# Performance work log

Hardware: AMD Instinct MI355X
Metric: run time of the kernel (lower is better)

The kernel has to match this reference:

```python
import jax, jax.numpy as jnp
import numpy as np

EPS = 1e-6

def _rmsnorm(x, w):
    # x: [..., Dh]
    inv = jax.lax.rsqrt(jnp.mean(x * x, axis=-1, keepdims=True) + EPS)
    return x * inv * w

def _apply_rope(x, rope):
    # x: [B, H, L, Dh], rope: [L, Dh//2, 2]
    L = x.shape[-2]
    cos = rope[:L, :, 0]  # [L, Dh//2]
    sin = rope[:L, :, 1]
    x_even = x[..., 0::2]
    x_odd = x[..., 1::2]
    rot = jnp.stack([x_even * cos - x_odd * sin,
                     x_even * sin + x_odd * cos], axis=-1)  # [B,H,L,Dh//2,2]
    return rot.reshape(*x.shape[:-1], -1)


def setup_inputs() -> dict:
    key = jax.random.key(0)
    ks = jax.random.split(key, 4)
    B, L, D = 2, 2048, 1024
    H, Dh = 16, 64
    x = jax.random.normal(ks[0], (B, L, D), dtype=jnp.float32)
    rope = jax.random.normal(ks[1], (L, Dh // 2, 2), dtype=jnp.float32)
    w_qkv = jax.random.normal(ks[2], (3 * D, D), dtype=jnp.float32) * (1.0 / np.sqrt(D))
    w_proj = jax.random.normal(ks[3], (D, D), dtype=jnp.float32) * (1.0 / np.sqrt(D))
    q_norm_w = jnp.ones((Dh,), dtype=jnp.float32)
    k_norm_w = jnp.ones((Dh,), dtype=jnp.float32)
    return {"x": x, "rope": rope, "w_qkv": w_qkv, "w_proj": w_proj,
            "q_norm_w": q_norm_w, "k_norm_w": k_norm_w}


def reference(x, rope, w_qkv, w_proj, q_norm_w, k_norm_w):
    B, L, D = x.shape
    H = 16
    Dh = D // H
    qkv = jnp.einsum('bld,ed->ble', x, w_qkv).reshape(B, L, 3, H, Dh)
    qkv = jnp.transpose(qkv, (2, 0, 3, 1, 4))  # [3, B, H, L, Dh]
    q, k, v = qkv[0], qkv[1], qkv[2]
    q = _rmsnorm(q, q_norm_w)
    k = _rmsnorm(k, k_norm_w)
    q = _apply_rope(q, rope)
    k = _apply_rope(k, rope)
    scale = 1.0 / np.sqrt(Dh)
    scores = jnp.einsum('bhqd,bhkd->bhqk', q, k) * scale
    attn = jax.nn.softmax(scores, axis=-1)
    out = jnp.einsum('bhqk,bhkd->bhqd', attn, v)  # [B,H,L,Dh]
    out = jnp.transpose(out, (0, 2, 1, 3)).reshape(B, L, D)
    return jnp.einsum('bld,ed->ble', out, w_proj)
```

## Files before the change

### kernel.cpp

```cpp
#include <hip/hip_runtime.h>

typedef unsigned short u16;
typedef unsigned int u32;
typedef __bf16 bf16x8 __attribute__((ext_vector_type(8)));
typedef float f32x4 __attribute__((ext_vector_type(4)));

#define L_SEQ 2048
#define NH 16
#define DH 64
#define D_MODEL 1024
#define ATT_SHIFT2 14.426950408889634f

__device__ __forceinline__ u16 f2bf(float f) {
  union { float f; u32 u; } v; v.f = f;
  u32 u = v.u;
  return (u16)((u + 0x7fffu + ((u >> 16) & 1u)) >> 16);
}
__device__ __forceinline__ float bf2f(u16 b) {
  union { u32 u; float f; } v; v.u = ((u32)b) << 16;
  return v.f;
}
__device__ __forceinline__ u32 pk2(float lo_val, float hi_val) {
  union { float f; u32 u; } a, b;
  a.f = hi_val; b.f = lo_val;
  return __builtin_amdgcn_perm(a.u + 0x8000u, b.u + 0x8000u, 0x07060302u);
}
__device__ __forceinline__ u32 pk2t(float lo_val, float hi_val) {
  union { float f; u32 u; } a, b;
  a.f = hi_val; b.f = lo_val;
  return __builtin_amdgcn_perm(a.u, b.u, 0x07060302u);
}
__device__ __forceinline__ bf16x8 ld8(const u16* p) {
  union { uint4 u; bf16x8 b; } v;
  v.u = *(const uint4*)p;
  return v.b;
}
__device__ __forceinline__ f32x4 fzero4() { f32x4 z = {0.f, 0.f, 0.f, 0.f}; return z; }

__device__ __forceinline__ float fexp2(float x) {
#if __has_builtin(__builtin_amdgcn_exp2f)
  return __builtin_amdgcn_exp2f(x);
#else
  return __expf(x * 0.6931471805599453f);
#endif
}

__device__ __forceinline__ void gll16(const u16* g, u16* l) {
  __builtin_amdgcn_global_load_lds((const __attribute__((address_space(1))) u32*)g,
                                   (__attribute__((address_space(3))) u32*)l, 16, 0, 0);
}

__global__ __launch_bounds__(256) void cvt_all(const float* __restrict__ x,
                                               const float* __restrict__ wqkv,
                                               const float* __restrict__ wproj,
                                               u16* __restrict__ xb,
                                               u16* __restrict__ wqkvb,
                                               u16* __restrict__ wprojb) {
  int i = blockIdx.x * 256 + threadIdx.x;
  const float* s;
  u16* d;
  int off;
  if (i < 1048576)      { s = x;     d = xb;     off = i; }
  else if (i < 1835008) { s = wqkv;  d = wqkvb;  off = i - 1048576; }
  else                  { s = wproj; d = wprojb; off = i - 1835008; }
  float4 v = ((const float4*)s)[off];
  ((ushort4*)d)[off] = make_ushort4(f2bf(v.x), f2bf(v.y), f2bf(v.z), f2bf(v.w));
}

__global__ __launch_bounds__(256) void gemm_qkv(const u16* __restrict__ A,
                                                const u16* __restrict__ B,
                                                u16* __restrict__ qb,
                                                u16* __restrict__ kb,
                                                u16* __restrict__ vtb) {
  __shared__ u16 smem[16384];
  u16* As = smem;
  u16* Bs = smem + 8192;
  const int t = threadIdx.x;
  const int lane = t & 63, wv = t >> 6;
  const int col = lane & 15, quad = lane >> 4;
  const int wr = wv >> 1, wc = wv & 1;
  const int m0 = blockIdx.y * 128, n0 = blockIdx.x * 128;

  f32x4 acc[4][4];
#pragma unroll
  for (int i = 0; i < 4; ++i)
#pragma unroll
    for (int j = 0; j < 4; ++j) acc[i][j] = fzero4();

  for (int kt = 0; kt < 1024; kt += 64) {
    __syncthreads();
#pragma unroll
    for (int it = 0; it < 4; ++it) {
      int id0 = it * 256 + wv * 64;
      int id = id0 + lane;
      int row = id >> 3, cs = id & 7;
      int csrc = cs ^ (row & 7);
      gll16(A + (size_t)(m0 + row) * 1024 + kt + csrc * 8, As + (size_t)id0 * 8);
      gll16(B + (size_t)(n0 + row) * 1024 + kt + csrc * 8, Bs + (size_t)id0 * 8);
    }
    __syncthreads();
#pragma unroll
    for (int c = 0; c < 2; ++c) {
      bf16x8 af[4], bfv[4];
#pragma unroll
      for (int f = 0; f < 4; ++f) {
        int r = wr * 64 + f * 16 + col;
        af[f] = ld8(&As[(r * 8 + ((c * 4 + quad) ^ (r & 7))) * 8]);
        int rb = wc * 64 + f * 16 + col;
        bfv[f] = ld8(&Bs[(rb * 8 + ((c * 4 + quad) ^ (rb & 7))) * 8]);
      }
#pragma unroll
      for (int i = 0; i < 4; ++i)
#pragma unroll
        for (int j = 0; j < 4; ++j)
          acc[i][j] = __builtin_amdgcn_mfma_f32_16x16x32_bf16(af[i], bfv[j], acc[i][j], 0, 0, 0);
    }
  }

  const int region = n0 >> 10;
  if (region < 2) {
    u16* dst = region ? kb : qb;
#pragma unroll
    for (int i = 0; i < 4; ++i) {
      int gr = m0 + wr * 64 + i * 16 + quad * 4;
      int b = gr >> 11, l = gr & 2047;
#pragma unroll
      for (int j = 0; j < 4; ++j) {
        int gc = (n0 & 1023) + wc * 64 + j * 16 + col;
        int h = gc >> 6, dh = gc & 63;
        size_t base = ((size_t)(b * NH + h) * L_SEQ + l) * DH + dh;
#pragma unroll
        for (int r = 0; r < 4; ++r)
          dst[base + (size_t)r * DH] = f2bf(acc[i][j][r]);
      }
    }
  } else {
    __syncthreads();
#pragma unroll
    for (int i = 0; i < 4; ++i) {
      int m_l = wr * 64 + i * 16 + quad * 4;
#pragma unroll
      for (int j = 0; j < 4; ++j) {
        int n_l = wc * 64 + j * 16 + col;
        int ta = n_l * 128 + (m_l ^ ((n_l & 15) << 3));
        *(uint2*)(smem + ta) = make_uint2(pk2(acc[i][j][0], acc[i][j][1]),
                                          pk2(acc[i][j][2], acc[i][j][3]));
      }
    }
    __syncthreads();
    const int b = m0 >> 11, lbase = m0 & 2047;
    const int n_l = t >> 1, mh = (t & 1) * 64;
    const int gc = (n0 - 2048) + n_l;
    const int h = gc >> 6, dh = gc & 63;
    u16* vrow = vtb + ((size_t)(b * NH + h) * DH + dh) * L_SEQ + lbase + mh;
#pragma unroll
    for (int c2 = 0; c2 < 8; ++c2) {
      int m = mh + c2 * 8;
      uint4 v = *(const uint4*)(smem + n_l * 128 + (m ^ ((n_l & 15) << 3)));
      *(uint4*)(vrow + c2 * 8) = v;
    }
  }
}

__global__ __launch_bounds__(256) void qk_norm_rope(u16* __restrict__ qb,
                                                    u16* __restrict__ kb,
                                                    const float* __restrict__ rope,
                                                    const float* __restrict__ qw,
                                                    const float* __restrict__ kw) {
  const int t = threadIdx.x;
  const int lane = t & 63, wv = t >> 6;
  const int gid = blockIdx.x * 4 + wv;
  const int l = gid & (L_SEQ - 1);
  const int b = gid >> 11;
  const int lg = lane & 7;
  const float QSCALE = 0.125f * 1.4426950408889634f;

  float wqv[8], wkv[8], rp[8];
  {
    float4 a = *(const float4*)(qw + lg * 8);
    float4 c = *(const float4*)(qw + lg * 8 + 4);
    wqv[0]=a.x; wqv[1]=a.y; wqv[2]=a.z; wqv[3]=a.w; wqv[4]=c.x; wqv[5]=c.y; wqv[6]=c.z; wqv[7]=c.w;
    a = *(const float4*)(kw + lg * 8);
    c = *(const float4*)(kw + lg * 8 + 4);
    wkv[0]=a.x; wkv[1]=a.y; wkv[2]=a.z; wkv[3]=a.w; wkv[4]=c.x; wkv[5]=c.y; wkv[6]=c.z; wkv[7]=c.w;
    a = *(const float4*)(rope + (size_t)l * 64 + lg * 8);
    c = *(const float4*)(rope + (size_t)l * 64 + lg * 8 + 4);
    rp[0]=a.x; rp[1]=a.y; rp[2]=a.z; rp[3]=a.w; rp[4]=c.x; rp[5]=c.y; rp[6]=c.z; rp[7]=c.w;
  }

#pragma unroll
  for (int i = 0; i < 2; ++i) {
    const int head = i * 8 + (lane >> 3);
    size_t addr = ((size_t)(b * NH + head) * L_SEQ + l) * DH + lg * 8;
    bf16x8 q8 = ld8(qb + addr);
    bf16x8 k8 = ld8(kb + addr);
    float q[8], k[8];
#pragma unroll
    for (int j = 0; j < 8; ++j) { q[j] = (float)q8[j]; k[j] = (float)k8[j]; }
    float sq = 0.f, sk = 0.f;
#pragma unroll
    for (int j = 0; j < 8; ++j) { sq += q[j] * q[j]; sk += k[j] * k[j]; }
    sq += __shfl_xor(sq, 1); sq += __shfl_xor(sq, 2); sq += __shfl_xor(sq, 4);
    sk += __shfl_xor(sk, 1); sk += __shfl_xor(sk, 2); sk += __shfl_xor(sk, 4);
    float qi = rsqrtf(sq * (1.f / 64.f) + 1e-6f);
    float ki = rsqrtf(sk * (1.f / 64.f) + 1e-6f);

    float rq[8], rk[8];
#pragma unroll
    for (int j = 0; j < 4; ++j) {
      float cs = rp[2 * j], sn = rp[2 * j + 1];
      float qe = q[2 * j] * qi * wqv[2 * j], qo = q[2 * j + 1] * qi * wqv[2 * j + 1];
      float ke = k[2 * j] * ki * wkv[2 * j], ko = k[2 * j + 1] * ki * wkv[2 * j + 1];
      rq[2 * j]     = (qe * cs - qo * sn) * QSCALE;
      rq[2 * j + 1] = (qe * sn + qo * cs) * QSCALE;
      rk[2 * j]     = ke * cs - ko * sn;
      rk[2 * j + 1] = ke * sn + ko * cs;
    }
    *(uint4*)(qb + addr) = make_uint4(pk2(rq[0], rq[1]), pk2(rq[2], rq[3]),
                                      pk2(rq[4], rq[5]), pk2(rq[6], rq[7]));
    *(uint4*)(kb + addr) = make_uint4(pk2(rk[0], rk[1]), pk2(rk[2], rk[3]),
                                      pk2(rk[4], rk[5]), pk2(rk[6], rk[7]));
  }
}

__global__ __launch_bounds__(256) void attn_flash(const u16* __restrict__ qb,
                                                  const u16* __restrict__ kb,
                                                  const u16* __restrict__ vtb,
                                                  u16* __restrict__ po,
                                                  float* __restrict__ pl) {
  __shared__ u16 ldsK[4096];
  __shared__ u16 ldsV[4096];
  __shared__ u16 ldsP[8192];
  const int t = threadIdx.x;
  const int lane = t & 63, wv = t >> 6;
  const int col = lane & 15, quad = lane >> 4;
  const int bh = blockIdx.x;
  const int half = blockIdx.z;
  const int q0 = blockIdx.y * 128 + wv * 32;

  const u16* kbase = kb + ((size_t)bh * L_SEQ + half * 1024) * DH;
  const u16* vbase = vtb + (size_t)bh * DH * L_SEQ + half * 1024;

  bf16x8 qfrag[2][2];
#pragma unroll
  for (int qf = 0; qf < 2; ++qf)
#pragma unroll
    for (int c = 0; c < 2; ++c)
      qfrag[qf][c] = ld8(qb + ((size_t)bh * L_SEQ + q0 + qf * 16 + col) * DH + c * 32 + quad * 8);

  f32x4 o[2][4];
#pragma unroll
  for (int qf = 0; qf < 2; ++qf)
#pragma unroll
    for (int nf = 0; nf < 4; ++nf) o[qf][nf] = fzero4();
  float lrow[2] = {0.f, 0.f};

  u16* pb = &ldsP[wv * 2048];

  for (int tt = 0; tt < 16; ++tt) {
    __syncthreads();
    {
      const int kt = tt * 64;
#pragma unroll
      for (int it = 0; it < 2; ++it) {
        int id0 = it * 256 + wv * 64;
        int id = id0 + lane;
        int row = id >> 3, cs = id & 7, csrc = cs ^ (row & 7);
        gll16(kbase + (size_t)(kt + row) * DH + csrc * 8, ldsK + (size_t)id0 * 8);
        gll16(vbase + (size_t)row * L_SEQ + kt + csrc * 8, ldsV + (size_t)id0 * 8);
      }
    }
    __syncthreads();

    f32x4 s[2][4];
#pragma unroll
    for (int qf = 0; qf < 2; ++qf)
#pragma unroll
      for (int mf = 0; mf < 4; ++mf) s[qf][mf] = fzero4();
#pragma unroll
    for (int c = 0; c < 2; ++c) {
#pragma unroll
      for (int mf = 0; mf < 4; ++mf) {
        int kr = mf * 16 + col;
        bf16x8 kf = ld8(&ldsK[kr * 64 + (((c * 4 + quad) ^ (kr & 7)) * 8)]);
#pragma unroll
        for (int qf = 0; qf < 2; ++qf)
          s[qf][mf] = __builtin_amdgcn_mfma_f32_16x16x32_bf16(kf, qfrag[qf][c], s[qf][mf], 0, 0, 0);
      }
    }

#pragma unroll
    for (int qf = 0; qf < 2; ++qf) {
      float ts = 0.f;
#pragma unroll
      for (int mf = 0; mf < 4; ++mf)
#pragma unroll
        for (int r = 0; r < 4; ++r) {
          float e = fexp2(s[qf][mf][r] - ATT_SHIFT2);
          s[qf][mf][r] = e;
          ts += e;
        }
      lrow[qf] += ts;
      const int q = qf * 16 + col;
#pragma unroll
      for (int mf = 0; mf < 4; ++mf) {
        int slot = q * 8 + ((2 * mf + (quad >> 1)) ^ (q & 7));
        *(uint2*)(pb + slot * 8 + (quad & 1) * 4) =
            make_uint2(pk2t(s[qf][mf][0], s[qf][mf][1]), pk2t(s[qf][mf][2], s[qf][mf][3]));
      }
    }

#pragma unroll
    for (int c = 0; c < 2; ++c) {
      bf16x8 pa[2];
#pragma unroll
      for (int qf = 0; qf < 2; ++qf) {
        const int q = qf * 16 + col;
        pa[qf] = ld8(pb + (q * 8 + ((c * 4 + quad) ^ (q & 7))) * 8);
      }
#pragma unroll
      for (int nf = 0; nf < 4; ++nf) {
        int vr = nf * 16 + col;
        bf16x8 vf = ld8(&ldsV[vr * 64 + (((c * 4 + quad) ^ (vr & 7)) * 8)]);
#pragma unroll
        for (int qf = 0; qf < 2; ++qf)
          o[qf][nf] = __builtin_amdgcn_mfma_f32_16x16x32_bf16(pa[qf], vf, o[qf][nf], 0, 0, 0);
      }
    }
  }

  u16* pob = po + (size_t)(half * 32 + bh) * L_SEQ * DH;
#pragma unroll
  for (int qf = 0; qf < 2; ++qf) {
    lrow[qf] += __shfl_xor(lrow[qf], 16);
    lrow[qf] += __shfl_xor(lrow[qf], 32);
    if (quad == 0)
      pl[(size_t)(half * 32 + bh) * L_SEQ + q0 + qf * 16 + col] = lrow[qf];
#pragma unroll
    for (int nf = 0; nf < 4; ++nf)
#pragma unroll
      for (int r = 0; r < 4; ++r)
        pob[(size_t)(q0 + qf * 16 + quad * 4 + r) * DH + nf * 16 + col] = f2bf(o[qf][nf][r]);
  }
}

__global__ __launch_bounds__(256) void gemm2_cmb(const u16* __restrict__ po,
                                                 const float* __restrict__ pl,
                                                 const u16* __restrict__ B,
                                                 float* __restrict__ out) {
  __shared__ u16 As[64 * 64];
  __shared__ u16 Bs[128 * 64];
  const int t = threadIdx.x;
  const int lane = t & 63, wv = t >> 6;
  const int col = lane & 15, quad = lane >> 4;
  const int wr = wv >> 1, wc = wv & 1;
  const int m0 = blockIdx.y * 64, n0 = blockIdx.x * 128;
  const int srow = t >> 2, kc0 = (t & 3) * 2;
  const int m = m0 + srow, bb = m >> 11, ll = m & 2047;

  f32x4 acc[2][4];
#pragma unroll
  for (int i = 0; i < 2; ++i)
#pragma unroll
    for (int j = 0; j < 4; ++j) acc[i][j] = fzero4();

  for (int kt = 0; kt < 1024; kt += 64) {
    __syncthreads();
    {
      int h = kt >> 6;
      size_t lidx = (size_t)(bb * 16 + h) * L_SEQ + ll;
      float inv = 1.0f / (pl[lidx] + pl[65536 + lidx]);
      size_t rowoff = lidx * 64;
#pragma unroll
      for (int i = 0; i < 2; ++i) {
        int kc = kc0 + i;
        uint4 a0 = *(const uint4*)(po + rowoff + kc * 8);
        uint4 a1 = *(const uint4*)(po + 4194304 + rowoff + kc * 8);
        union { uint4 u; u16 s[8]; } ua, ub;
        ua.u = a0; ub.u = a1;
        float r[8];
#pragma unroll
        for (int j = 0; j < 8; ++j) r[j] = (bf2f(ua.s[j]) + bf2f(ub.s[j])) * inv;
        uint4 pk = make_uint4(pk2(r[0], r[1]), pk2(r[2], r[3]), pk2(r[4], r[5]), pk2(r[6], r[7]));
        int slot = srow * 8 + (kc ^ (srow & 7));
        *(uint4*)(As + slot * 8) = pk;
      }
    }
#pragma unroll
    for (int it = 0; it < 4; ++it) {
      int id0 = it * 256 + wv * 64;
      int id = id0 + lane;
      int row = id >> 3, cs = id & 7, csrc = cs ^ (row & 7);
      gll16(B + (size_t)(n0 + row) * 1024 + kt + csrc * 8, Bs + (size_t)id0 * 8);
    }
    __syncthreads();
#pragma unroll
    for (int c = 0; c < 2; ++c) {
      bf16x8 af[2], bfv[4];
#pragma unroll
      for (int f = 0; f < 2; ++f) {
        int r = wr * 32 + f * 16 + col;
        af[f] = ld8(&As[(r * 8 + ((c * 4 + quad) ^ (r & 7))) * 8]);
      }
#pragma unroll
      for (int f = 0; f < 4; ++f) {
        int rb = wc * 64 + f * 16 + col;
        bfv[f] = ld8(&Bs[(rb * 8 + ((c * 4 + quad) ^ (rb & 7))) * 8]);
      }
#pragma unroll
      for (int i = 0; i < 2; ++i)
#pragma unroll
        for (int j = 0; j < 4; ++j)
          acc[i][j] = __builtin_amdgcn_mfma_f32_16x16x32_bf16(af[i], bfv[j], acc[i][j], 0, 0, 0);
    }
  }
#pragma unroll
  for (int i = 0; i < 2; ++i) {
    int gr = m0 + wr * 32 + i * 16 + quad * 4;
#pragma unroll
    for (int j = 0; j < 4; ++j) {
      int gc = n0 + wc * 64 + j * 16 + col;
#pragma unroll
      for (int r = 0; r < 4; ++r)
        out[(size_t)(gr + r) * D_MODEL + gc] = acc[i][j][r];
    }
  }
}

extern "C" void kernel_launch(void* const* d_in, const int* in_sizes, int n_in,
                              void* d_out, int out_size, void* d_ws, size_t ws_size,
                              hipStream_t stream) {
  const float* x     = (const float*)d_in[0];
  const float* rope  = (const float*)d_in[1];
  const float* wqkv  = (const float*)d_in[2];
  const float* wproj = (const float*)d_in[3];
  const float* qnw   = (const float*)d_in[4];
  const float* knw   = (const float*)d_in[5];
  float* out = (float*)d_out;
  char* ws = (char*)d_ws;

  u16* xb     = (u16*)(ws + 0);
  u16* wqkvb  = (u16*)(ws + 8388608);
  u16* wprojb = (u16*)(ws + 14680064);
  u16* qb     = (u16*)(ws + 16777216);
  u16* kb     = (u16*)(ws + 25165824);
  u16* vtb    = (u16*)(ws + 33554432);
  u16* po     = (u16*)(ws + 41943040);
  float* pl   = (float*)(ws + 58720256);

  cvt_all<<<8192, 256, 0, stream>>>(x, wqkv, wproj, xb, wqkvb, wprojb);

  gemm_qkv<<<dim3(24, 32), 256, 0, stream>>>(xb, wqkvb, qb, kb, vtb);

  qk_norm_rope<<<1024, 256, 0, stream>>>(qb, kb, rope, qnw, knw);

  attn_flash<<<dim3(32, 16, 2), 256, 0, stream>>>(qb, kb, vtb, po, pl);

  gemm2_cmb<<<dim3(8, 64), 256, 0, stream>>>(po, pl, wprojb, out);
}
```

Before: 214.9 us.

## Fuse QK RMSNorm and RoPE into QKV GEMM epilogue; enlarge attention query tile

Moves the per-head RMSNorm, RoPE rotation and query scaling into the QKV GEMM epilogue using cross-lane shuffles. This removes the separate qk_norm_rope kernel and its extra read and write of Q and K. The attention kernel now handles 64 queries per wave instead of 32, so each K/V tile loaded into LDS is reused across more queries. It also restructures the score/exp loop per key fragment, which doubles the P buffer in LDS and raises register pressure. The epilogue now does scalar bf16 stores with per-element rope loads, which may be less efficient than before.

```diff
diff --git a/kernel.cpp b/kernel.cpp
--- a/kernel.cpp
+++ b/kernel.cpp
@@ -10,6 +10,7 @@
 #define DH 64
 #define D_MODEL 1024
 #define ATT_SHIFT2 14.426950408889634f
+#define QSCALE_LOG2E 0.18033688011112042f
 
 __device__ __forceinline__ u16 f2bf(float f) {
   union { float f; u32 u; } v; v.f = f;
@@ -69,6 +70,9 @@
 
 __global__ __launch_bounds__(256) void gemm_qkv(const u16* __restrict__ A,
                                                 const u16* __restrict__ B,
+                                                const float* __restrict__ rope,
+                                                const float* __restrict__ qw,
+                                                const float* __restrict__ kw,
                                                 u16* __restrict__ qb,
                                                 u16* __restrict__ kb,
                                                 u16* __restrict__ vtb) {
@@ -119,19 +123,36 @@
 
   const int region = n0 >> 10;
   if (region < 2) {
+    const float* w = region ? kw : qw;
     u16* dst = region ? kb : qb;
+    const float scale = region ? 1.0f : QSCALE_LOG2E;
+    const int h = ((n0 & 1023) >> 6) + wc;
+    float wloc[4];
+#pragma unroll
+    for (int j = 0; j < 4; ++j) wloc[j] = w[j * 16 + col];
 #pragma unroll
     for (int i = 0; i < 4; ++i) {
-      int gr = m0 + wr * 64 + i * 16 + quad * 4;
-      int b = gr >> 11, l = gr & 2047;
-#pragma unroll
-      for (int j = 0; j < 4; ++j) {
-        int gc = (n0 & 1023) + wc * 64 + j * 16 + col;
-        int h = gc >> 6, dh = gc & 63;
-        size_t base = ((size_t)(b * NH + h) * L_SEQ + l) * DH + dh;
-#pragma unroll
-        for (int r = 0; r < 4; ++r)
-          dst[base + (size_t)r * DH] = f2bf(acc[i][j][r]);
+#pragma unroll
+      for (int r = 0; r < 4; ++r) {
+        float v0 = acc[i][0][r], v1 = acc[i][1][r], v2 = acc[i][2][r], v3 = acc[i][3][r];
+        float ss = v0 * v0 + v1 * v1 + v2 * v2 + v3 * v3;
+        ss += __shfl_xor(ss, 1); ss += __shfl_xor(ss, 2);
+        ss += __shfl_xor(ss, 4); ss += __shfl_xor(ss, 8);
+        float inv = rsqrtf(ss * (1.f / 64.f) + 1e-6f);
+        int gr = m0 + wr * 64 + i * 16 + quad * 4 + r;
+        int b = gr >> 11, l = gr & 2047;
+        const float2* rope2 = (const float2*)rope + (size_t)l * 32;
+        size_t obase = ((size_t)(b * NH + h) * L_SEQ + l) * DH;
+        float vv[4] = {v0, v1, v2, v3};
+#pragma unroll
+        for (int j = 0; j < 4; ++j) {
+          float val = vv[j] * inv * wloc[j];
+          float part = __shfl_xor(val, 1);
+          float2 cs = rope2[j * 8 + (col >> 1)];
+          float outv = (lane & 1) ? (part * cs.y + val * cs.x)
+                                  : (val * cs.x - part * cs.y);
+          dst[obase + j * 16 + col] = f2bf(outv * scale);
+        }
       }
     }
   } else {
@@ -159,67 +180,6 @@
       uint4 v = *(const uint4*)(smem + n_l * 128 + (m ^ ((n_l & 15) << 3)));
       *(uint4*)(vrow + c2 * 8) = v;
     }
-  }
-}
-
-__global__ __launch_bounds__(256) void qk_norm_rope(u16* __restrict__ qb,
-                                                    u16* __restrict__ kb,
-                                                    const float* __restrict__ rope,
-                                                    const float* __restrict__ qw,
-                                                    const float* __restrict__ kw) {
-  const int t = threadIdx.x;
-  const int lane = t & 63, wv = t >> 6;
-  const int gid = blockIdx.x * 4 + wv;
-  const int l = gid & (L_SEQ - 1);
-  const int b = gid >> 11;
-  const int lg = lane & 7;
-  const float QSCALE = 0.125f * 1.4426950408889634f;
-
-  float wqv[8], wkv[8], rp[8];
-  {
-    float4 a = *(const float4*)(qw + lg * 8);
-    float4 c = *(const float4*)(qw + lg * 8 + 4);
-    wqv[0]=a.x; wqv[1]=a.y; wqv[2]=a.z; wqv[3]=a.w; wqv[4]=c.x; wqv[5]=c.y; wqv[6]=c.z; wqv[7]=c.w;
-    a = *(const float4*)(kw + lg * 8);
-    c = *(const float4*)(kw + lg * 8 + 4);
-    wkv[0]=a.x; wkv[1]=a.y; wkv[2]=a.z; wkv[3]=a.w; wkv[4]=c.x; wkv[5]=c.y; wkv[6]=c.z; wkv[7]=c.w;
-    a = *(const float4*)(rope + (size_t)l * 64 + lg * 8);
-    c = *(const float4*)(rope + (size_t)l * 64 + lg * 8 + 4);
-    rp[0]=a.x; rp[1]=a.y; rp[2]=a.z; rp[3]=a.w; rp[4]=c.x; rp[5]=c.y; rp[6]=c.z; rp[7]=c.w;
-  }
-
-#pragma unroll
-  for (int i = 0; i < 2; ++i) {
-    const int head = i * 8 + (lane >> 3);
-    size_t addr = ((size_t)(b * NH + head) * L_SEQ + l) * DH + lg * 8;
-    bf16x8 q8 = ld8(qb + addr);
-    bf16x8 k8 = ld8(kb + addr);
-    float q[8], k[8];
-#pragma unroll
-    for (int j = 0; j < 8; ++j) { q[j] = (float)q8[j]; k[j] = (float)k8[j]; }
-    float sq = 0.f, sk = 0.f;
-#pragma unroll
-    for (int j = 0; j < 8; ++j) { sq += q[j] * q[j]; sk += k[j] * k[j]; }
-    sq += __shfl_xor(sq, 1); sq += __shfl_xor(sq, 2); sq += __shfl_xor(sq, 4);
-    sk += __shfl_xor(sk, 1); sk += __shfl_xor(sk, 2); sk += __shfl_xor(sk, 4);
-    float qi = rsqrtf(sq * (1.f / 64.f) + 1e-6f);
-    float ki = rsqrtf(sk * (1.f / 64.f) + 1e-6f);
-
-    float rq[8], rk[8];
-#pragma unroll
-    for (int j = 0; j < 4; ++j) {
-      float cs = rp[2 * j], sn = rp[2 * j + 1];
-      float qe = q[2 * j] * qi * wqv[2 * j], qo = q[2 * j + 1] * qi * wqv[2 * j + 1];
-      float ke = k[2 * j] * ki * wkv[2 * j], ko = k[2 * j + 1] * ki * wkv[2 * j + 1];
-      rq[2 * j]     = (qe * cs - qo * sn) * QSCALE;
-      rq[2 * j + 1] = (qe * sn + qo * cs) * QSCALE;
-      rk[2 * j]     = ke * cs - ko * sn;
-      rk[2 * j + 1] = ke * sn + ko * cs;
-    }
-    *(uint4*)(qb + addr) = make_uint4(pk2(rq[0], rq[1]), pk2(rq[2], rq[3]),
-                                      pk2(rq[4], rq[5]), pk2(rq[6], rq[7]));
-    *(uint4*)(kb + addr) = make_uint4(pk2(rk[0], rk[1]), pk2(rk[2], rk[3]),
-                                      pk2(rk[4], rk[5]), pk2(rk[6], rk[7]));
   }
 }
 
@@ -230,32 +190,34 @@
                                                   float* __restrict__ pl) {
   __shared__ u16 ldsK[4096];
   __shared__ u16 ldsV[4096];
-  __shared__ u16 ldsP[8192];
+  __shared__ u16 ldsP[16384];
   const int t = threadIdx.x;
   const int lane = t & 63, wv = t >> 6;
   const int col = lane & 15, quad = lane >> 4;
   const int bh = blockIdx.x;
   const int half = blockIdx.z;
-  const int q0 = blockIdx.y * 128 + wv * 32;
+  const int q0 = blockIdx.y * 256 + wv * 64;
 
   const u16* kbase = kb + ((size_t)bh * L_SEQ + half * 1024) * DH;
   const u16* vbase = vtb + (size_t)bh * DH * L_SEQ + half * 1024;
 
-  bf16x8 qfrag[2][2];
-#pragma unroll
-  for (int qf = 0; qf < 2; ++qf)
+  bf16x8 qfrag[4][2];
+#pragma unroll
+  for (int qf = 0; qf < 4; ++qf)
 #pragma unroll
     for (int c = 0; c < 2; ++c)
       qfrag[qf][c] = ld8(qb + ((size_t)bh * L_SEQ + q0 + qf * 16 + col) * DH + c * 32 + quad * 8);
 
-  f32x4 o[2][4];
-#pragma unroll
-  for (int qf = 0; qf < 2; ++qf)
+  f32x4 o[4][4];
+#pragma unroll
+  for (int qf = 0; qf < 4; ++qf)
 #pragma unroll
     for (int nf = 0; nf < 4; ++nf) o[qf][nf] = fzero4();
-  float lrow[2] = {0.f, 0.f};
-
-  u16* pb = &ldsP[wv * 2048];
+  float lrow[4] = {0.f, 0.f, 0.f, 0.f};
+
+  u16* pb = &ldsP[wv * 4096];
+  const int kc_w = (quad >> 1);
+  const int sub = (quad & 1) * 4;
 
   for (int tt = 0; tt < 16; ++tt) {
     __syncthreads();
@@ -272,49 +234,36 @@
     }
     __syncthreads();
 
-    f32x4 s[2][4];
-#pragma unroll
-    for (int qf = 0; qf < 2; ++qf)
-#pragma unroll
-      for (int mf = 0; mf < 4; ++mf) s[qf][mf] = fzero4();
+#pragma unroll
+    for (int mf = 0; mf < 4; ++mf) {
+      const int kr = mf * 16 + col;
+      bf16x8 kf0 = ld8(&ldsK[kr * 64 + (((0 + quad) ^ (kr & 7)) * 8)]);
+      bf16x8 kf1 = ld8(&ldsK[kr * 64 + (((4 + quad) ^ (kr & 7)) * 8)]);
+      f32x4 s[4];
+#pragma unroll
+      for (int qf = 0; qf < 4; ++qf) {
+        s[qf] = __builtin_amdgcn_mfma_f32_16x16x32_bf16(kf0, qfrag[qf][0], fzero4(), 0, 0, 0);
+        s[qf] = __builtin_amdgcn_mfma_f32_16x16x32_bf16(kf1, qfrag[qf][1], s[qf], 0, 0, 0);
+      }
+      const int kc = mf * 2 + kc_w;
+#pragma unroll
+      for (int qf = 0; qf < 4; ++qf) {
+        float e0 = fexp2(s[qf][0] - ATT_SHIFT2);
+        float e1 = fexp2(s[qf][1] - ATT_SHIFT2);
+        float e2 = fexp2(s[qf][2] - ATT_SHIFT2);
+        float e3 = fexp2(s[qf][3] - ATT_SHIFT2);
+        lrow[qf] += (e0 + e1) + (e2 + e3);
+        const int q = qf * 16 + col;
+        const int slot = q * 8 + (kc ^ (q & 7));
+        *(uint2*)(pb + slot * 8 + sub) = make_uint2(pk2t(e0, e1), pk2t(e2, e3));
+      }
+    }
+
 #pragma unroll
     for (int c = 0; c < 2; ++c) {
-#pragma unroll
-      for (int mf = 0; mf < 4; ++mf) {
-        int kr = mf * 16 + col;
-        bf16x8 kf = ld8(&ldsK[kr * 64 + (((c * 4 + quad) ^ (kr & 7)) * 8)]);
-#pragma unroll
-        for (int qf = 0; qf < 2; ++qf)
-          s[qf][mf] = __builtin_amdgcn_mfma_f32_16x16x32_bf16(kf, qfrag[qf][c], s[qf][mf], 0, 0, 0);
-      }
-    }
-
-#pragma unroll
-    for (int qf = 0; qf < 2; ++qf) {
-      float ts = 0.f;
-#pragma unroll
-      for (int mf = 0; mf < 4; ++mf)
-#pragma unroll
-        for (int r = 0; r < 4; ++r) {
-          float e = fexp2(s[qf][mf][r] - ATT_SHIFT2);
-          s[qf][mf][r] = e;
-          ts += e;
-        }
-      lrow[qf] += ts;
-      const int q = qf * 16 + col;
-#pragma unroll
-      for (int mf = 0; mf < 4; ++mf) {
-        int slot = q * 8 + ((2 * mf + (quad >> 1)) ^ (q & 7));
-        *(uint2*)(pb + slot * 8 + (quad & 1) * 4) =
-            make_uint2(pk2t(s[qf][mf][0], s[qf][mf][1]), pk2t(s[qf][mf][2], s[qf][mf][3]));
-      }
-    }
-
-#pragma unroll
-    for (int c = 0; c < 2; ++c) {
-      bf16x8 pa[2];
-#pragma unroll
-      for (int qf = 0; qf < 2; ++qf) {
+      bf16x8 pa[4];
+#pragma unroll
+      for (int qf = 0; qf < 4; ++qf) {
         const int q = qf * 16 + col;
         pa[qf] = ld8(pb + (q * 8 + ((c * 4 + quad) ^ (q & 7))) * 8);
       }
@@ -323,7 +272,7 @@
         int vr = nf * 16 + col;
         bf16x8 vf = ld8(&ldsV[vr * 64 + (((c * 4 + quad) ^ (vr & 7)) * 8)]);
 #pragma unroll
-        for (int qf = 0; qf < 2; ++qf)
+        for (int qf = 0; qf < 4; ++qf)
           o[qf][nf] = __builtin_amdgcn_mfma_f32_16x16x32_bf16(pa[qf], vf, o[qf][nf], 0, 0, 0);
       }
     }
@@ -331,7 +280,7 @@
 
   u16* pob = po + (size_t)(half * 32 + bh) * L_SEQ * DH;
 #pragma unroll
-  for (int qf = 0; qf < 2; ++qf) {
+  for (int qf = 0; qf < 4; ++qf) {
     lrow[qf] += __shfl_xor(lrow[qf], 16);
     lrow[qf] += __shfl_xor(lrow[qf], 32);
     if (quad == 0)
@@ -450,11 +399,9 @@
 
   cvt_all<<<8192, 256, 0, stream>>>(x, wqkv, wproj, xb, wqkvb, wprojb);
 
-  gemm_qkv<<<dim3(24, 32), 256, 0, stream>>>(xb, wqkvb, qb, kb, vtb);
-
-  qk_norm_rope<<<1024, 256, 0, stream>>>(qb, kb, rope, qnw, knw);
-
-  attn_flash<<<dim3(32, 16, 2), 256, 0, stream>>>(qb, kb, vtb, po, pl);
+  gemm_qkv<<<dim3(24, 32), 256, 0, stream>>>(xb, wqkvb, rope, qnw, knw, qb, kb, vtb);
+
+  attn_flash<<<dim3(32, 8, 2), 256, 0, stream>>>(qb, kb, vtb, po, pl);
 
   gemm2_cmb<<<dim3(8, 64), 256, 0, stream>>>(po, pl, wprojb, out);
 }
```

Result: faster. 208.0 us (-3.2%).
